# Optimization experiments

Measured on AMD Instinct MI355X. Metric: run time of the kernel, lower is better.

## Reference

```python
import jax, jax.numpy as jnp
import numpy as np


def _quat_to_rot(q):
    # q: [B,4] (w,x,y,z); normalize as the torch code does when norm != 1
    q = q / jnp.linalg.norm(q, axis=-1, keepdims=True)
    w, x, y, z = q[:, 0], q[:, 1], q[:, 2], q[:, 3]
    r00 = 1 - 2 * y**2 - 2 * z**2
    r01 = 2 * x * y - 2 * z * w
    r02 = 2 * x * z + 2 * y * w
    r10 = 2 * x * y + 2 * z * w
    r11 = 1 - 2 * x**2 - 2 * z**2
    r12 = 2 * y * z - 2 * x * w
    r20 = 2 * x * z - 2 * y * w
    r21 = 2 * y * z + 2 * x * w
    r22 = 1 - 2 * x**2 - 2 * y**2
    R = jnp.stack([
        jnp.stack([r00, r01, r02], axis=-1),
        jnp.stack([r10, r11, r12], axis=-1),
        jnp.stack([r20, r21, r22], axis=-1),
    ], axis=-2)  # [B,3,3]
    return R


def setup_inputs() -> dict:
    key = jax.random.key(0)
    k1, k2, k3, k4 = jax.random.split(key, 4)
    B, N = 32, 262144
    return {
        "pcd_mis": jax.random.normal(k1, (B, N, 3), dtype=jnp.float32),
        "T_mis": jax.random.normal(k2, (B, 4, 4), dtype=jnp.float32),
        "delta_q_pred": jax.random.normal(k3, (B, 4), dtype=jnp.float32),
        "delta_t_pred": jax.random.normal(k4, (B, 3), dtype=jnp.float32),
    }


def reference(pcd_mis, T_mis, delta_q_pred, delta_t_pred):
    B = delta_q_pred.shape[0]
    R = _quat_to_rot(delta_q_pred)                      # [B,3,3]
    t = delta_t_pred[:, :, None]                        # [B,3,1]
    top = jnp.concatenate([R, t], axis=-1)              # [B,3,4]
    bottom = jnp.broadcast_to(
        jnp.array([0.0, 0.0, 0.0, 1.0], dtype=pcd_mis.dtype), (B, 1, 4))
    delta_T = jnp.concatenate([top, bottom], axis=-2)   # [B,4,4]
    inv_T = jnp.linalg.inv(delta_T)                     # [B,4,4]
    batch_T_pred = jnp.einsum('bij,bjk->bik', inv_T, T_mis)  # [B,4,4]
    # homogeneous point transform: only first 3 output rows are kept
    # new = (inv_T @ [p;1])[:3] = p @ Rinv^T + tinv
    pcd_new = jnp.einsum('bij,bnj->bni', inv_T[:, :3, :3], pcd_mis) \
        + inv_T[:, None, :3, 3]                          # [B,N,3]
    return (batch_T_pred, pcd_new)
```

## Files before the change

kernel.cpp:

```cpp
#include <hip/hip_runtime.h>
#include <math.h>

struct Inv {
    float i00, i01, i02, it0;
    float i10, i11, i12, it1;
    float i20, i21, i22, it2;
};

__device__ __forceinline__ Inv make_inv(const float* __restrict__ q,
                                        const float* __restrict__ t, int b) {
    float w = q[b * 4 + 0], x = q[b * 4 + 1], y = q[b * 4 + 2], z = q[b * 4 + 3];
    float inv_n = 1.0f / sqrtf(w * w + x * x + y * y + z * z);
    w *= inv_n; x *= inv_n; y *= inv_n; z *= inv_n;
    float R00 = 1.f - 2.f * y * y - 2.f * z * z;
    float R01 = 2.f * x * y - 2.f * z * w;
    float R02 = 2.f * x * z + 2.f * y * w;
    float R10 = 2.f * x * y + 2.f * z * w;
    float R11 = 1.f - 2.f * x * x - 2.f * z * z;
    float R12 = 2.f * y * z - 2.f * x * w;
    float R20 = 2.f * x * z - 2.f * y * w;
    float R21 = 2.f * y * z + 2.f * x * w;
    float R22 = 1.f - 2.f * x * x - 2.f * y * y;
    float t0 = t[b * 3 + 0], t1 = t[b * 3 + 1], t2 = t[b * 3 + 2];
    Inv v;
    v.i00 = R00; v.i01 = R10; v.i02 = R20; v.it0 = -(R00 * t0 + R10 * t1 + R20 * t2);
    v.i10 = R01; v.i11 = R11; v.i12 = R21; v.it1 = -(R01 * t0 + R11 * t1 + R21 * t2);
    v.i20 = R02; v.i21 = R12; v.i22 = R22; v.it2 = -(R02 * t0 + R12 * t1 + R22 * t2);
    return v;
}

__device__ __forceinline__ void xf(const Inv& M, float px, float py, float pz,
                                   float& ox, float& oy, float& oz) {
    ox = fmaf(M.i00, px, fmaf(M.i01, py, fmaf(M.i02, pz, M.it0)));
    oy = fmaf(M.i10, px, fmaf(M.i11, py, fmaf(M.i12, pz, M.it1)));
    oz = fmaf(M.i20, px, fmaf(M.i21, py, fmaf(M.i22, pz, M.it2)));
}

__global__ __launch_bounds__(256) void realign_fused_kernel(
        const float4* __restrict__ pcd,
        const float* __restrict__ T_mis,
        const float* __restrict__ q,
        const float* __restrict__ t,
        float* __restrict__ out_mat,
        float4* __restrict__ out_pcd,
        int f4_per_batch) {
    __shared__ float4 smem[768];
    const int b = blockIdx.y;
    const int tid = threadIdx.x;
    const size_t chunk = (size_t)b * (size_t)f4_per_batch + (size_t)blockIdx.x * 768u;

    float4 r0 = pcd[chunk + tid];
    float4 r1 = pcd[chunk + 256 + tid];
    float4 r2 = pcd[chunk + 512 + tid];

    const Inv M = make_inv(q, t, b);

    smem[tid]       = r0;
    smem[256 + tid] = r1;
    smem[512 + tid] = r2;

    if (blockIdx.x == 0 && tid < 16) {
        const int i = tid >> 2;
        const int j = tid & 3;
        const float* Tb = T_mis + b * 16;
        float val;
        if (i < 3) {
            float a0, a1, a2, it;
            if (i == 0)      { a0 = M.i00; a1 = M.i01; a2 = M.i02; it = M.it0; }
            else if (i == 1) { a0 = M.i10; a1 = M.i11; a2 = M.i12; it = M.it1; }
            else             { a0 = M.i20; a1 = M.i21; a2 = M.i22; it = M.it2; }
            val = fmaf(a0, Tb[0 * 4 + j],
                  fmaf(a1, Tb[1 * 4 + j],
                  fmaf(a2, Tb[2 * 4 + j],
                       it * Tb[3 * 4 + j])));
        } else {
            val = Tb[3 * 4 + j];
        }
        out_mat[b * 16 + tid] = val;
    }

    __syncthreads();

    float4 v0 = smem[3 * tid + 0];
    float4 v1 = smem[3 * tid + 1];
    float4 v2 = smem[3 * tid + 2];
    float4 o0, o1, o2;
    xf(M, v0.x, v0.y, v0.z, o0.x, o0.y, o0.z);
    xf(M, v0.w, v1.x, v1.y, o0.w, o1.x, o1.y);
    xf(M, v1.z, v1.w, v2.x, o1.z, o1.w, o2.x);
    xf(M, v2.y, v2.z, v2.w, o2.y, o2.z, o2.w);
    smem[3 * tid + 0] = o0;
    smem[3 * tid + 1] = o1;
    smem[3 * tid + 2] = o2;

    __syncthreads();

    out_pcd[chunk + tid]       = smem[tid];
    out_pcd[chunk + 256 + tid] = smem[256 + tid];
    out_pcd[chunk + 512 + tid] = smem[512 + tid];
}

extern "C" void kernel_launch(void* const* d_in, const int* in_sizes, int n_in,
                              void* d_out, int out_size, void* d_ws, size_t ws_size,
                              hipStream_t stream) {
    const float* pcd   = (const float*)d_in[0];
    const float* T_mis = (const float*)d_in[1];
    const float* q     = (const float*)d_in[2];
    const float* t     = (const float*)d_in[3];
    float* out = (float*)d_out;

    const int B = in_sizes[2] / 4;
    const long long N = (long long)in_sizes[0] / (3LL * B);
    const int f4_per_batch = (int)(3 * N / 4);
    const int blocks_x = f4_per_batch / 768;

    dim3 grid(blocks_x, B);
    realign_fused_kernel<<<grid, 256, 0, stream>>>(
        (const float4*)pcd, T_mis, q, t,
        out, (float4*)(out + B * 16), f4_per_batch);
}
```

Baseline: 182.0 us.

## Make blocks loop over several chunks and prefetch the next chunk during compute

Each block now handles four strided chunks per batch instead of one, with a quarter as many blocks. While it transforms and stores the current chunk it loads the next chunk into registers. The __syncthreads calls are replaced by inline asm barriers that wait only on LDS counters, so outstanding global loads are not drained at each barrier. The aim is to overlap memory latency and cut block launch overhead, at the cost of fewer resident blocks and more registers for a purely bandwidth-bound kernel.

New measurement: 185.0 us. No clear change (+1.6%).

```diff
diff --git a/kernel.cpp b/kernel.cpp
--- a/kernel.cpp
+++ b/kernel.cpp
@@ -36,6 +36,10 @@
     oz = fmaf(M.i20, px, fmaf(M.i21, py, fmaf(M.i22, pz, M.it2)));
 }
 
+__device__ __forceinline__ void bar_lgkm() {
+    asm volatile("s_waitcnt lgkmcnt(0)\n\ts_barrier" ::: "memory");
+}
+
 __global__ __launch_bounds__(256) void realign_fused_kernel(
         const float4* __restrict__ pcd,
         const float* __restrict__ T_mis,
@@ -43,21 +47,18 @@
         const float* __restrict__ t,
         float* __restrict__ out_mat,
         float4* __restrict__ out_pcd,
-        int f4_per_batch) {
+        int f4_per_batch, int stride_f4, int n_iters) {
     __shared__ float4 smem[768];
     const int b = blockIdx.y;
     const int tid = threadIdx.x;
-    const size_t chunk = (size_t)b * (size_t)f4_per_batch + (size_t)blockIdx.x * 768u;
 
-    float4 r0 = pcd[chunk + tid];
-    float4 r1 = pcd[chunk + 256 + tid];
-    float4 r2 = pcd[chunk + 512 + tid];
+    size_t base = (size_t)b * (size_t)f4_per_batch + (size_t)blockIdx.x * 768u;
+
+    float4 r0 = pcd[base + tid];
+    float4 r1 = pcd[base + 256 + tid];
+    float4 r2 = pcd[base + 512 + tid];
 
     const Inv M = make_inv(q, t, b);
-
-    smem[tid]       = r0;
-    smem[256 + tid] = r1;
-    smem[512 + tid] = r2;
 
     if (blockIdx.x == 0 && tid < 16) {
         const int i = tid >> 2;
@@ -79,25 +80,49 @@
         out_mat[b * 16 + tid] = val;
     }
 
-    __syncthreads();
+    smem[tid]       = r0;
+    smem[256 + tid] = r1;
+    smem[512 + tid] = r2;
+    bar_lgkm();
 
-    float4 v0 = smem[3 * tid + 0];
-    float4 v1 = smem[3 * tid + 1];
-    float4 v2 = smem[3 * tid + 2];
-    float4 o0, o1, o2;
-    xf(M, v0.x, v0.y, v0.z, o0.x, o0.y, o0.z);
-    xf(M, v0.w, v1.x, v1.y, o0.w, o1.x, o1.y);
-    xf(M, v1.z, v1.w, v2.x, o1.z, o1.w, o2.x);
-    xf(M, v2.y, v2.z, v2.w, o2.y, o2.z, o2.w);
-    smem[3 * tid + 0] = o0;
-    smem[3 * tid + 1] = o1;
-    smem[3 * tid + 2] = o2;
+    for (int it = 0; it < n_iters; ++it) {
+        float4 n0{}, n1{}, n2{};
+        const bool has_next = (it + 1 < n_iters);
+        if (has_next) {
+            const size_t nb = base + (size_t)stride_f4;
+            n0 = pcd[nb + tid];
+            n1 = pcd[nb + 256 + tid];
+            n2 = pcd[nb + 512 + tid];
+        }
 
-    __syncthreads();
+        float4 v0 = smem[3 * tid + 0];
+        float4 v1 = smem[3 * tid + 1];
+        float4 v2 = smem[3 * tid + 2];
+        float4 o0, o1, o2;
+        xf(M, v0.x, v0.y, v0.z, o0.x, o0.y, o0.z);
+        xf(M, v0.w, v1.x, v1.y, o0.w, o1.x, o1.y);
+        xf(M, v1.z, v1.w, v2.x, o1.z, o1.w, o2.x);
+        xf(M, v2.y, v2.z, v2.w, o2.y, o2.z, o2.w);
+        smem[3 * tid + 0] = o0;
+        smem[3 * tid + 1] = o1;
+        smem[3 * tid + 2] = o2;
+        bar_lgkm();
 
-    out_pcd[chunk + tid]       = smem[tid];
-    out_pcd[chunk + 256 + tid] = smem[256 + tid];
-    out_pcd[chunk + 512 + tid] = smem[512 + tid];
+        float4 s0 = smem[tid];
+        float4 s1 = smem[256 + tid];
+        float4 s2 = smem[512 + tid];
+        out_pcd[base + tid]       = s0;
+        out_pcd[base + 256 + tid] = s1;
+        out_pcd[base + 512 + tid] = s2;
+        if (has_next) {
+            smem[tid]       = n0;
+            smem[256 + tid] = n1;
+            smem[512 + tid] = n2;
+        }
+        bar_lgkm();
+
+        base += (size_t)stride_f4;
+    }
 }
 
 extern "C" void kernel_launch(void* const* d_in, const int* in_sizes, int n_in,
@@ -112,10 +137,15 @@
     const int B = in_sizes[2] / 4;
     const long long N = (long long)in_sizes[0] / (3LL * B);
     const int f4_per_batch = (int)(3 * N / 4);
-    const int blocks_x = f4_per_batch / 768;
+    const int chunks = f4_per_batch / 768;
+
+    int iters = 4;
+    if (chunks % 4 != 0) iters = (chunks % 2 == 0) ? 2 : 1;
+    const int blocks_x = chunks / iters;
+    const int stride_f4 = blocks_x * 768;
 
     dim3 grid(blocks_x, B);
     realign_fused_kernel<<<grid, 256, 0, stream>>>(
         (const float4*)pcd, T_mis, q, t,
-        out, (float4*)(out + B * 16), f4_per_batch);
+        out, (float4*)(out + B * 16), f4_per_batch, stride_f4, iters);
 }
```
